# Performance work log

Measured on AMD Instinct MI355X. Metric: run time of the kernel, lower is better.

Reference implementation:

```python
import jax, jax.numpy as jnp
import numpy as np

NEG_FILL = jnp.finfo(jnp.float32).min  # stands in for tf.float64.min (overflows to -inf in f32)


def setup_inputs() -> dict:
    key = jax.random.key(0)
    k0, k1, k2, k3, k4 = jax.random.split(key, 5)
    B, N, E, D = 4, 4096, 1024, 256
    STD = 0.05  # tf.random_normal_initializer default stddev
    inputs = jax.random.normal(k0, (B, N, E), dtype=jnp.float32)
    Wq = STD * jax.random.normal(k1, (E, D), dtype=jnp.float32)
    Wk = STD * jax.random.normal(k2, (E, D), dtype=jnp.float32)
    Wvdown = STD * jax.random.normal(k3, (E, D), dtype=jnp.float32)
    Wvup = STD * jax.random.normal(k4, (D, E), dtype=jnp.float32)
    return {"inputs": inputs, "Wq": Wq, "Wk": Wk, "Wvdown": Wvdown, "Wvup": Wvup}


def reference(inputs, Wq, Wk, Wvdown, Wvup):
    B, N, E = inputs.shape
    D = Wq.shape[1]
    Q = inputs @ Wq                                   # [B, N, D]
    K = inputs @ Wk                                   # [B, N, D]
    score = jnp.einsum("bqd,bkd->bqk", Q, K)          # [B, N, N]
    score = score / jnp.sqrt(jnp.float32(D))
    # tf.linalg.band_part(score, -1, 0): keep lower triangle (causal)
    causal = jnp.tril(jnp.ones((N, N), dtype=bool))
    score = jnp.where(causal, score, 0.0)
    # original quirk: any exactly-zero entry (including masked ones) -> huge negative
    score = jnp.where(score != 0, score, NEG_FILL)
    attn = jax.nn.softmax(score, axis=-1)             # [B, N, N]
    V = inputs @ (Wvdown @ Wvup)                      # low-rank value proj, [B, N, E]
    return attn @ V                                   # [B, N, E]
```

## Files before the change

### kernel.cpp

```cpp
#include <hip/hip_runtime.h>
#include <hip/hip_bf16.h>


typedef __hip_bfloat16 bf16;
typedef __bf16 bf16x4 __attribute__((ext_vector_type(4)));
typedef __bf16 bf16x8 __attribute__((ext_vector_type(8)));
typedef float f32x4 __attribute__((ext_vector_type(4)));

#define BK 32
#define HALF_BYTES 8192

__device__ __forceinline__ void gload_lds16(const bf16* g, bf16* l) {
    __builtin_amdgcn_global_load_lds(
        (const __attribute__((address_space(1))) unsigned int*)g,
        (__attribute__((address_space(3))) unsigned int*)l, 16, 0, 0);
}

__device__ __forceinline__ void zero_acc(f32x4 acc[4][4]) {
#pragma unroll
    for (int mi = 0; mi < 4; ++mi)
#pragma unroll
        for (int ni = 0; ni < 4; ++ni) {
            f32x4 zf = {0.f, 0.f, 0.f, 0.f};
            acc[mi][ni] = zf;
        }
}

__device__ __forceinline__ void compute_step(const bf16* As, const bf16* Bs,
                                             int cur, int mrow, int nrow,
                                             int koff, f32x4 acc[4][4]) {
    const bf16* Ar = (const bf16*)((const char*)As + cur * HALF_BYTES);
    const bf16* Br = (const bf16*)((const char*)Bs + cur * HALF_BYTES);
    bf16x8 af[4], bfr[4];
#pragma unroll
    for (int mi = 0; mi < 4; ++mi)
        af[mi] = *(const bf16x8*)(Ar + (mrow + mi * 16) * BK + koff);
#pragma unroll
    for (int ni = 0; ni < 4; ++ni)
        bfr[ni] = *(const bf16x8*)(Br + (nrow + ni * 16) * BK + koff);
#pragma unroll
    for (int mi = 0; mi < 4; ++mi)
#pragma unroll
        for (int ni = 0; ni < 4; ++ni)
            acc[mi][ni] = __builtin_amdgcn_mfma_f32_16x16x32_bf16(
                af[mi], bfr[ni], acc[mi][ni], 0, 0, 0);
}

__device__ __forceinline__ void mm_tile(const bf16* __restrict__ Ablk,
                                        const bf16* __restrict__ Bblk,
                                        int lda, int ldb, int kiters,
                                        bf16* As, bf16* Bs, f32x4 acc[4][4]) {
    const int tid  = threadIdx.x;
    const int wave = tid >> 6;
    const int lane = tid & 63;

    const int F0 = wave * 2048 + lane * 16;
    const int F1 = F0 + 1024;
    const int r0 = F0 >> 6, c0 = (F0 & 63) >> 1;
    const int r1 = F1 >> 6, c1 = (F1 & 63) >> 1;
    const bf16* ga0 = Ablk + (size_t)r0 * lda + c0;
    const bf16* ga1 = Ablk + (size_t)r1 * lda + c1;
    const bf16* gb0 = Bblk + (size_t)r0 * ldb + c0;
    const bf16* gb1 = Bblk + (size_t)r1 * ldb + c1;

    const int waveM = wave >> 1, waveN = wave & 1;
    const int mrow = waveM * 64 + (lane & 15);
    const int nrow = waveN * 64 + (lane & 15);
    const int koff = (lane >> 4) * 8;

    gload_lds16(ga0, (bf16*)((char*)As + F0));
    gload_lds16(ga1, (bf16*)((char*)As + F1));
    gload_lds16(gb0, (bf16*)((char*)Bs + F0));
    gload_lds16(gb1, (bf16*)((char*)Bs + F1));
    ga0 += BK; ga1 += BK; gb0 += BK; gb1 += BK;

    int cur = 0;
    for (int it = 0; it < kiters - 1; ++it) {
        const int nxt = cur ^ 1;
        char* Ad = (char*)As + nxt * HALF_BYTES;
        char* Bd = (char*)Bs + nxt * HALF_BYTES;
        gload_lds16(ga0, (bf16*)(Ad + F0));
        gload_lds16(ga1, (bf16*)(Ad + F1));
        gload_lds16(gb0, (bf16*)(Bd + F0));
        gload_lds16(gb1, (bf16*)(Bd + F1));
        ga0 += BK; ga1 += BK; gb0 += BK; gb1 += BK;

        __builtin_amdgcn_sched_barrier(0);
        asm volatile("s_waitcnt vmcnt(4)" ::: "memory");
        __builtin_amdgcn_sched_barrier(0);
        __builtin_amdgcn_s_barrier();
        __builtin_amdgcn_sched_barrier(0);

        compute_step(As, Bs, cur, mrow, nrow, koff, acc);

        __builtin_amdgcn_sched_barrier(0);
        asm volatile("s_waitcnt lgkmcnt(0)" ::: "memory");
        __builtin_amdgcn_sched_barrier(0);
        __builtin_amdgcn_s_barrier();
        __builtin_amdgcn_sched_barrier(0);
        cur = nxt;
    }

    __builtin_amdgcn_sched_barrier(0);
    asm volatile("s_waitcnt vmcnt(0)" ::: "memory");
    __builtin_amdgcn_sched_barrier(0);
    __builtin_amdgcn_s_barrier();
    __builtin_amdgcn_sched_barrier(0);
    compute_step(As, Bs, cur, mrow, nrow, koff, acc);
}

__global__ __launch_bounds__(256, 2) void k_gemm_plain(
    const bf16* __restrict__ A, long long aBatch,
    const bf16* __restrict__ BT, long long bBatch,
    bf16* __restrict__ C, long long cBatch,
    int lda, int ldb, int ldc, int kiters) {
    __shared__ __align__(16) bf16 As[2 * 128 * BK];
    __shared__ __align__(16) bf16 Bs[2 * 128 * BK];
    const int nBase = blockIdx.x * 128;
    const int mBase = blockIdx.y * 128;
    const int z = blockIdx.z;
    const bf16* Ab = A + (size_t)z * aBatch + (size_t)mBase * lda;
    const bf16* Bb = BT + (size_t)z * bBatch + (size_t)nBase * ldb;

    f32x4 acc[4][4];
    zero_acc(acc);
    mm_tile(Ab, Bb, lda, ldb, kiters, As, Bs, acc);

    const int tid = threadIdx.x, wave = tid >> 6, lane = tid & 63;
    const int waveM = wave >> 1, waveN = wave & 1;
    const int quad = lane >> 4, cno = lane & 15;
    bf16* Cb = C + (size_t)z * cBatch;
#pragma unroll
    for (int mi = 0; mi < 4; ++mi) {
        int row0 = mBase + waveM * 64 + mi * 16 + quad * 4;
#pragma unroll
        for (int ni = 0; ni < 4; ++ni) {
            int col = nBase + waveN * 64 + ni * 16 + cno;
#pragma unroll
            for (int r = 0; r < 4; ++r)
                Cb[(size_t)(row0 + r) * ldc + col] = __float2bfloat16(acc[mi][ni][r]);
        }
    }
}

#define P_BATCH 8650752ll
__global__ __launch_bounds__(256, 2) void k_score(
    const bf16* __restrict__ Qm, const bf16* __restrict__ Km,
    bf16* __restrict__ P, float* __restrict__ lsum) {
    const int f = blockIdx.x, b = blockIdx.z;
    int qt = (int)((sqrtf(8.f * (float)f + 1.f) - 1.f) * 0.5f);
    while ((qt + 1) * (qt + 2) / 2 <= f) ++qt;
    while (qt * (qt + 1) / 2 > f) --qt;
    const int kt = f - qt * (qt + 1) / 2;

    __shared__ __align__(16) bf16 As[2 * 128 * BK];
    __shared__ __align__(16) bf16 Bs[2 * 128 * BK];

    const bf16* Ab = Qm + ((size_t)b * 4096 + (size_t)qt * 128) * 256;
    const bf16* Bb = Km + ((size_t)b * 4096 + (size_t)kt * 128) * 256;

    f32x4 acc[4][4];
    zero_acc(acc);
    mm_tile(Ab, Bb, 256, 256, 256 / BK, As, Bs, acc);

    const int tid = threadIdx.x, wave = tid >> 6, lane = tid & 63;
    const int waveM = wave >> 1, waveN = wave & 1;
    const int quad = lane >> 4, cno = lane & 15;
    const int pitch = (qt + 1) * 128;
    bf16* Pb = P + b * P_BATCH + (size_t)16384 * (qt * (qt + 1) / 2);
    float* lb = lsum + b * 4096;
#pragma unroll
    for (int mi = 0; mi < 4; ++mi) {
        const int lq0 = waveM * 64 + mi * 16 + quad * 4;
        float rs[4] = {0.f, 0.f, 0.f, 0.f};
#pragma unroll
        for (int ni = 0; ni < 4; ++ni) {
            const int cn = waveN * 64 + ni * 16 + cno;
            const int gk = kt * 128 + cn;
#pragma unroll
            for (int r = 0; r < 4; ++r) {
                const int gq = qt * 128 + lq0 + r;
                float s = acc[mi][ni][r] * 0.0625f;
                float p = (gk <= gq && s != 0.0f) ? __expf(s) : 0.0f;
                bf16 pb = __float2bfloat16(p);
                Pb[(size_t)(lq0 + r) * pitch + gk] = pb;
                rs[r] += __bfloat162float(pb);
            }
        }
#pragma unroll
        for (int r = 0; r < 4; ++r) {
            float v = rs[r];
            v += __shfl_xor(v, 1);
            v += __shfl_xor(v, 2);
            v += __shfl_xor(v, 4);
            v += __shfl_xor(v, 8);
            if (cno == 0) atomicAdd(&lb[qt * 128 + lq0 + r], v);
        }
    }
}

__global__ __launch_bounds__(256, 2) void k_pv(
    const bf16* __restrict__ P, const bf16* __restrict__ VT,
    const float* __restrict__ lsum, float* __restrict__ Out) {
    __shared__ __align__(16) bf16 As[2 * 128 * BK];
    __shared__ __align__(16) bf16 Bs[2 * 128 * BK];
    const int l = blockIdx.x;
    const int dv = l >> 7;
    const int w = l & 127;
    const int b = w >> 5;
    const int u = w & 31;
    const int x = u & 7;
    const int k = u >> 3;
    const int m = (k + (dv >> 1)) & 3;
    const int qt = (m == 0) ? x : (m == 1) ? (15 - x)
                 : (m == 2) ? (16 + x) : (31 - x);
    const int dvBase = dv * 128;
    const int tid = threadIdx.x, wave = tid >> 6, lane = tid & 63;
    const int waveM = wave >> 1, waveN = wave & 1;
    const int quad = lane >> 4, cno = lane & 15;

    const bf16* Bb = VT + ((size_t)b * 1024 + dvBase) * 4096;
    float* Ob = Out + (size_t)b * 4096 * 1024;
    const float* lb = lsum + b * 4096;

    const int pitch = (qt + 1) * 128;
    const bf16* Ab = P + b * P_BATCH + (size_t)16384 * (qt * (qt + 1) / 2);

    f32x4 acc[4][4];
    zero_acc(acc);
    mm_tile(Ab, Bb, pitch, 4096, (qt + 1) * (128 / BK), As, Bs, acc);

#pragma unroll
    for (int mi = 0; mi < 4; ++mi) {
        const int lq0 = waveM * 64 + mi * 16 + quad * 4;
#pragma unroll
        for (int r = 0; r < 4; ++r) {
            const int gq = qt * 128 + lq0 + r;
            const float inv = 1.0f / lb[gq];
#pragma unroll
            for (int ni = 0; ni < 4; ++ni) {
                const int col = dvBase + waveN * 64 + ni * 16 + cno;
                Ob[(size_t)gq * 1024 + col] = acc[mi][ni][r] * inv;
            }
        }
    }
}

__global__ void k_cast(const float4* __restrict__ in, bf16* __restrict__ out,
                       int n4) {
    int i = blockIdx.x * 256 + threadIdx.x;
    if (i >= n4) return;
    float4 v = in[i];
    bf16x4 o;
    o[0] = (__bf16)v.x; o[1] = (__bf16)v.y; o[2] = (__bf16)v.z; o[3] = (__bf16)v.w;
    *(bf16x4*)(out + 4 * (size_t)i) = o;
}

__global__ void k_transpose(const float* __restrict__ in, bf16* __restrict__ out,
                            int n, int mask, int shift, int tstride) {
    int idx = blockIdx.x * 256 + threadIdx.x;
    if (idx >= n) return;
    out[idx] = __float2bfloat16(in[(size_t)(idx & mask) * tstride + (idx >> shift)]);
}

extern "C" void kernel_launch(void* const* d_in, const int* in_sizes, int n_in,
                              void* d_out, int out_size, void* d_ws, size_t ws_size,
                              hipStream_t stream) {
    const int B = 4, N = 4096, E = 1024, D = 256;
    const float* X   = (const float*)d_in[0];
    const float* Wq  = (const float*)d_in[1];
    const float* Wk  = (const float*)d_in[2];
    const float* Wvd = (const float*)d_in[3];
    const float* Wvu = (const float*)d_in[4];
    float* out = (float*)d_out;

    const long long MiB = 1ll << 20;
    char* ws = (char*)d_ws;
    bf16* Xb     = (bf16*)(ws);
    bf16* WqT    = (bf16*)(ws + 32 * MiB);
    bf16* WkT    = (bf16*)(ws + 32 * MiB + 524288);
    bf16* WvdT   = (bf16*)(ws + 32 * MiB + 1048576);
    bf16* WvupT  = (bf16*)(ws + 32 * MiB + 1572864);
    bf16* P      = (bf16*)(ws);
    bf16* Qm     = (bf16*)(ws + 66 * MiB);
    bf16* Km     = (bf16*)(ws + 74 * MiB);
    bf16* Vd     = (bf16*)(ws + 82 * MiB);
    bf16* VT     = (bf16*)(ws + 90 * MiB);
    float* lsum  = (float*)(ws + 122 * MiB);

    const int n4 = B * N * E / 4;
    k_cast<<<(n4 + 255) / 256, 256, 0, stream>>>((const float4*)X, Xb, n4);
    k_transpose<<<1024, 256, 0, stream>>>(Wq,  WqT,  E * D, 1023, 10, 256);
    k_transpose<<<1024, 256, 0, stream>>>(Wk,  WkT,  E * D, 1023, 10, 256);
    k_transpose<<<1024, 256, 0, stream>>>(Wvd, WvdT, E * D, 1023, 10, 256);
    k_transpose<<<1024, 256, 0, stream>>>(Wvu, WvupT, D * E, 255, 8, 1024);
    hipMemsetAsync(lsum, 0, (size_t)B * N * sizeof(float), stream);

    k_gemm_plain<<<dim3(D / 128, (B * N) / 128, 3), 256, 0, stream>>>(
        Xb, 0, WqT, (long long)D * E, Qm, (long long)B * N * D,
        E, E, D, E / BK);

    k_gemm_plain<<<dim3(N / 128, E / 128, B), 256, 0, stream>>>(
        WvupT, 0, Vd, (long long)N * D, VT, (long long)E * N,
        D, D, N, D / BK);

    k_score<<<dim3(528, 1, B), 256, 0, stream>>>(Qm, Km, P, lsum);

    k_pv<<<dim3(1024, 1, 1), 256, 0, stream>>>(P, VT, lsum, out);
}
```

Baseline: 331.6 us.

## Swizzle LDS tiles and add triple-buffered pipeline for PV GEMM

```diff
diff --git a/kernel.cpp b/kernel.cpp
--- a/kernel.cpp
+++ b/kernel.cpp
@@ -28,16 +28,16 @@
 
 __device__ __forceinline__ void compute_step(const bf16* As, const bf16* Bs,
                                              int cur, int mrow, int nrow,
-                                             int koff, f32x4 acc[4][4]) {
-    const bf16* Ar = (const bf16*)((const char*)As + cur * HALF_BYTES);
-    const bf16* Br = (const bf16*)((const char*)Bs + cur * HALF_BYTES);
+                                             int kswz, f32x4 acc[4][4]) {
+    const char* Ar = (const char*)As + cur * HALF_BYTES;
+    const char* Br = (const char*)Bs + cur * HALF_BYTES;
     bf16x8 af[4], bfr[4];
 #pragma unroll
     for (int mi = 0; mi < 4; ++mi)
-        af[mi] = *(const bf16x8*)(Ar + (mrow + mi * 16) * BK + koff);
+        af[mi] = *(const bf16x8*)(Ar + (mrow + mi * 16) * 64 + kswz);
 #pragma unroll
     for (int ni = 0; ni < 4; ++ni)
-        bfr[ni] = *(const bf16x8*)(Br + (nrow + ni * 16) * BK + koff);
+        bfr[ni] = *(const bf16x8*)(Br + (nrow + ni * 16) * 64 + kswz);
 #pragma unroll
     for (int mi = 0; mi < 4; ++mi)
 #pragma unroll
@@ -46,6 +46,7 @@
                 af[mi], bfr[ni], acc[mi][ni], 0, 0, 0);
 }
 
+template <int DEPTH>
 __device__ __forceinline__ void mm_tile(const bf16* __restrict__ Ablk,
                                         const bf16* __restrict__ Bblk,
                                         int lda, int ldb, int kiters,
@@ -56,8 +57,9 @@
 
     const int F0 = wave * 2048 + lane * 16;
     const int F1 = F0 + 1024;
-    const int r0 = F0 >> 6, c0 = (F0 & 63) >> 1;
-    const int r1 = F1 >> 6, c1 = (F1 & 63) >> 1;
+    const int r0 = F0 >> 6, r1 = F1 >> 6;
+    const int c0 = ((F0 & 63) ^ ((r0 & 3) << 4)) >> 1;
+    const int c1 = ((F1 & 63) ^ ((r1 & 3) << 4)) >> 1;
     const bf16* ga0 = Ablk + (size_t)r0 * lda + c0;
     const bf16* ga1 = Ablk + (size_t)r1 * lda + c1;
     const bf16* gb0 = Bblk + (size_t)r0 * ldb + c0;
@@ -66,39 +68,60 @@
     const int waveM = wave >> 1, waveN = wave & 1;
     const int mrow = waveM * 64 + (lane & 15);
     const int nrow = waveN * 64 + (lane & 15);
-    const int koff = (lane >> 4) * 8;
-
-    gload_lds16(ga0, (bf16*)((char*)As + F0));
-    gload_lds16(ga1, (bf16*)((char*)As + F1));
-    gload_lds16(gb0, (bf16*)((char*)Bs + F0));
-    gload_lds16(gb1, (bf16*)((char*)Bs + F1));
-    ga0 += BK; ga1 += BK; gb0 += BK; gb1 += BK;
+    const int kswz = (((lane >> 4) ^ (lane & 3)) << 4);
+
+#define STAGE_TO(buf)                                                        \
+    {                                                                        \
+        char* Ad = (char*)As + (buf) * HALF_BYTES;                           \
+        char* Bd = (char*)Bs + (buf) * HALF_BYTES;                           \
+        gload_lds16(ga0, (bf16*)(Ad + F0));                                  \
+        gload_lds16(ga1, (bf16*)(Ad + F1));                                  \
+        gload_lds16(gb0, (bf16*)(Bd + F0));                                  \
+        gload_lds16(gb1, (bf16*)(Bd + F1));                                  \
+        ga0 += BK; ga1 += BK; gb0 += BK; gb1 += BK;                          \
+    }
+
+    STAGE_TO(0);
+    if (DEPTH == 3) STAGE_TO(1);
 
     int cur = 0;
-    for (int it = 0; it < kiters - 1; ++it) {
-        const int nxt = cur ^ 1;
-        char* Ad = (char*)As + nxt * HALF_BYTES;
-        char* Bd = (char*)Bs + nxt * HALF_BYTES;
-        gload_lds16(ga0, (bf16*)(Ad + F0));
-        gload_lds16(ga1, (bf16*)(Ad + F1));
-        gload_lds16(gb0, (bf16*)(Bd + F0));
-        gload_lds16(gb1, (bf16*)(Bd + F1));
-        ga0 += BK; ga1 += BK; gb0 += BK; gb1 += BK;
-
+    int stg = DEPTH - 1;
+    for (int it = 0; it < kiters - (DEPTH - 1); ++it) {
+        STAGE_TO(stg);
+        stg = (stg + 1 == DEPTH) ? 0 : stg + 1;
+
+        __builtin_amdgcn_sched_barrier(0);
+        if constexpr (DEPTH == 2)
+            asm volatile("s_waitcnt vmcnt(4)" ::: "memory");
+        else
+            asm volatile("s_waitcnt vmcnt(8)" ::: "memory");
+        __builtin_amdgcn_sched_barrier(0);
+        __builtin_amdgcn_s_barrier();
+        __builtin_amdgcn_sched_barrier(0);
+
+        compute_step(As, Bs, cur, mrow, nrow, kswz, acc);
+
+        __builtin_amdgcn_sched_barrier(0);
+        asm volatile("s_waitcnt lgkmcnt(0)" ::: "memory");
+        __builtin_amdgcn_sched_barrier(0);
+        __builtin_amdgcn_s_barrier();
+        __builtin_amdgcn_sched_barrier(0);
+        cur = (cur + 1 == DEPTH) ? 0 : cur + 1;
+    }
+
+    if constexpr (DEPTH == 3) {
         __builtin_amdgcn_sched_barrier(0);
         asm volatile("s_waitcnt vmcnt(4)" ::: "memory");
         __builtin_amdgcn_sched_barrier(0);
         __builtin_amdgcn_s_barrier();
         __builtin_amdgcn_sched_barrier(0);
-
-        compute_step(As, Bs, cur, mrow, nrow, koff, acc);
-
+        compute_step(As, Bs, cur, mrow, nrow, kswz, acc);
         __builtin_amdgcn_sched_barrier(0);
         asm volatile("s_waitcnt lgkmcnt(0)" ::: "memory");
         __builtin_amdgcn_sched_barrier(0);
         __builtin_amdgcn_s_barrier();
         __builtin_amdgcn_sched_barrier(0);
-        cur = nxt;
+        cur = (cur + 1 == DEPTH) ? 0 : cur + 1;
     }
 
     __builtin_amdgcn_sched_barrier(0);
@@ -106,7 +129,8 @@
     __builtin_amdgcn_sched_barrier(0);
     __builtin_amdgcn_s_barrier();
     __builtin_amdgcn_sched_barrier(0);
-    compute_step(As, Bs, cur, mrow, nrow, koff, acc);
+    compute_step(As, Bs, cur, mrow, nrow, kswz, acc);
+#undef STAGE_TO
 }
 
 __global__ __launch_bounds__(256, 2) void k_gemm_plain(
@@ -124,7 +148,7 @@
 
     f32x4 acc[4][4];
     zero_acc(acc);
-    mm_tile(Ab, Bb, lda, ldb, kiters, As, Bs, acc);
+    mm_tile<2>(Ab, Bb, lda, ldb, kiters, As, Bs, acc);
 
     const int tid = threadIdx.x, wave = tid >> 6, lane = tid & 63;
     const int waveM = wave >> 1, waveN = wave & 1;
@@ -161,7 +185,7 @@
 
     f32x4 acc[4][4];
     zero_acc(acc);
-    mm_tile(Ab, Bb, 256, 256, 256 / BK, As, Bs, acc);
+    mm_tile<2>(Ab, Bb, 256, 256, 256 / BK, As, Bs, acc);
 
     const int tid = threadIdx.x, wave = tid >> 6, lane = tid & 63;
     const int waveM = wave >> 1, waveN = wave & 1;
@@ -202,8 +226,8 @@
 __global__ __launch_bounds__(256, 2) void k_pv(
     const bf16* __restrict__ P, const bf16* __restrict__ VT,
     const float* __restrict__ lsum, float* __restrict__ Out) {
-    __shared__ __align__(16) bf16 As[2 * 128 * BK];
-    __shared__ __align__(16) bf16 Bs[2 * 128 * BK];
+    __shared__ __align__(16) bf16 As[3 * 128 * BK];
+    __shared__ __align__(16) bf16 Bs[3 * 128 * BK];
     const int l = blockIdx.x;
     const int dv = l >> 7;
     const int w = l & 127;
@@ -228,7 +252,7 @@
 
     f32x4 acc[4][4];
     zero_acc(acc);
-    mm_tile(Ab, Bb, pitch, 4096, (qt + 1) * (128 / BK), As, Bs, acc);
+    mm_tile<3>(Ab, Bb, pitch, 4096, (qt + 1) * (128 / BK), As, Bs, acc);
 
 #pragma unroll
     for (int mi = 0; mi < 4; ++mi) {
```

New measurement: 369.1 us. +11.3%, slower.

## Load MFMA fragments directly from global memory in score and PV kernels

Applied to the files above, without the earlier changes.

```diff
diff --git a/kernel.cpp b/kernel.cpp
--- a/kernel.cpp
+++ b/kernel.cpp
@@ -26,24 +26,45 @@
         }
 }
 
-__device__ __forceinline__ void compute_step(const bf16* As, const bf16* Bs,
-                                             int cur, int mrow, int nrow,
-                                             int koff, f32x4 acc[4][4]) {
-    const bf16* Ar = (const bf16*)((const char*)As + cur * HALF_BYTES);
-    const bf16* Br = (const bf16*)((const char*)Bs + cur * HALF_BYTES);
-    bf16x8 af[4], bfr[4];
-#pragma unroll
-    for (int mi = 0; mi < 4; ++mi)
-        af[mi] = *(const bf16x8*)(Ar + (mrow + mi * 16) * BK + koff);
-#pragma unroll
-    for (int ni = 0; ni < 4; ++ni)
-        bfr[ni] = *(const bf16x8*)(Br + (nrow + ni * 16) * BK + koff);
-#pragma unroll
-    for (int mi = 0; mi < 4; ++mi)
-#pragma unroll
-        for (int ni = 0; ni < 4; ++ni)
-            acc[mi][ni] = __builtin_amdgcn_mfma_f32_16x16x32_bf16(
-                af[mi], bfr[ni], acc[mi][ni], 0, 0, 0);
+__device__ __forceinline__ void mm_tile_direct(const bf16* __restrict__ Ablk,
+                                               const bf16* __restrict__ Bblk,
+                                               int lda, int ldb, int kiters,
+                                               f32x4 acc[4][4]) {
+    const int tid  = threadIdx.x;
+    const int wave = tid >> 6;
+    const int lane = tid & 63;
+    const int waveM = wave >> 1, waveN = wave & 1;
+    const int mrow = waveM * 64 + (lane & 15);
+    const int nrow = waveN * 64 + (lane & 15);
+    const int koff = (lane >> 4) * 8;
+
+    const bf16* pa0 = Ablk + (size_t)(mrow +  0) * lda + koff;
+    const bf16* pa1 = Ablk + (size_t)(mrow + 16) * lda + koff;
+    const bf16* pa2 = Ablk + (size_t)(mrow + 32) * lda + koff;
+    const bf16* pa3 = Ablk + (size_t)(mrow + 48) * lda + koff;
+    const bf16* pb0 = Bblk + (size_t)(nrow +  0) * ldb + koff;
+    const bf16* pb1 = Bblk + (size_t)(nrow + 16) * ldb + koff;
+    const bf16* pb2 = Bblk + (size_t)(nrow + 32) * ldb + koff;
+    const bf16* pb3 = Bblk + (size_t)(nrow + 48) * ldb + koff;
+
+#pragma unroll 2
+    for (int it = 0; it < kiters; ++it) {
+        bf16x8 af[4], bfr[4];
+        af[0] = *(const bf16x8*)pa0; pa0 += BK;
+        af[1] = *(const bf16x8*)pa1; pa1 += BK;
+        af[2] = *(const bf16x8*)pa2; pa2 += BK;
+        af[3] = *(const bf16x8*)pa3; pa3 += BK;
+        bfr[0] = *(const bf16x8*)pb0; pb0 += BK;
+        bfr[1] = *(const bf16x8*)pb1; pb1 += BK;
+        bfr[2] = *(const bf16x8*)pb2; pb2 += BK;
+        bfr[3] = *(const bf16x8*)pb3; pb3 += BK;
+#pragma unroll
+        for (int mi = 0; mi < 4; ++mi)
+#pragma unroll
+            for (int ni = 0; ni < 4; ++ni)
+                acc[mi][ni] = __builtin_amdgcn_mfma_f32_16x16x32_bf16(
+                    af[mi], bfr[ni], acc[mi][ni], 0, 0, 0);
+    }
 }
 
 __device__ __forceinline__ void mm_tile(const bf16* __restrict__ Ablk,
@@ -68,22 +89,22 @@
     const int nrow = waveN * 64 + (lane & 15);
     const int koff = (lane >> 4) * 8;
 
-    gload_lds16(ga0, (bf16*)((char*)As + F0));
-    gload_lds16(ga1, (bf16*)((char*)As + F1));
-    gload_lds16(gb0, (bf16*)((char*)Bs + F0));
-    gload_lds16(gb1, (bf16*)((char*)Bs + F1));
-    ga0 += BK; ga1 += BK; gb0 += BK; gb1 += BK;
-
+#define STAGE_TO(buf)                                                        \
+    {                                                                        \
+        char* Ad = (char*)As + (buf) * HALF_BYTES;                           \
+        char* Bd = (char*)Bs + (buf) * HALF_BYTES;                           \
+        gload_lds16(ga0, (bf16*)(Ad + F0));                                  \
+        gload_lds16(ga1, (bf16*)(Ad + F1));                                  \
+        gload_lds16(gb0, (bf16*)(Bd + F0));                                  \
+        gload_lds16(gb1, (bf16*)(Bd + F1));                                  \
+        ga0 += BK; ga1 += BK; gb0 += BK; gb1 += BK;                          \
+    }
+
+    STAGE_TO(0);
     int cur = 0;
     for (int it = 0; it < kiters - 1; ++it) {
         const int nxt = cur ^ 1;
-        char* Ad = (char*)As + nxt * HALF_BYTES;
-        char* Bd = (char*)Bs + nxt * HALF_BYTES;
-        gload_lds16(ga0, (bf16*)(Ad + F0));
-        gload_lds16(ga1, (bf16*)(Ad + F1));
-        gload_lds16(gb0, (bf16*)(Bd + F0));
-        gload_lds16(gb1, (bf16*)(Bd + F1));
-        ga0 += BK; ga1 += BK; gb0 += BK; gb1 += BK;
+        STAGE_TO(nxt);
 
         __builtin_amdgcn_sched_barrier(0);
         asm volatile("s_waitcnt vmcnt(4)" ::: "memory");
@@ -91,7 +112,23 @@
         __builtin_amdgcn_s_barrier();
         __builtin_amdgcn_sched_barrier(0);
 
-        compute_step(As, Bs, cur, mrow, nrow, koff, acc);
+        {
+            const bf16* Ar = (const bf16*)((const char*)As + cur * HALF_BYTES);
+            const bf16* Br = (const bf16*)((const char*)Bs + cur * HALF_BYTES);
+            bf16x8 af[4], bfr[4];
+#pragma unroll
+            for (int mi = 0; mi < 4; ++mi)
+                af[mi] = *(const bf16x8*)(Ar + (mrow + mi * 16) * BK + koff);
+#pragma unroll
+            for (int ni = 0; ni < 4; ++ni)
+                bfr[ni] = *(const bf16x8*)(Br + (nrow + ni * 16) * BK + koff);
+#pragma unroll
+            for (int mi = 0; mi < 4; ++mi)
+#pragma unroll
+                for (int ni = 0; ni < 4; ++ni)
+                    acc[mi][ni] = __builtin_amdgcn_mfma_f32_16x16x32_bf16(
+                        af[mi], bfr[ni], acc[mi][ni], 0, 0, 0);
+        }
 
         __builtin_amdgcn_sched_barrier(0);
         asm volatile("s_waitcnt lgkmcnt(0)" ::: "memory");
@@ -106,7 +143,24 @@
     __builtin_amdgcn_sched_barrier(0);
     __builtin_amdgcn_s_barrier();
     __builtin_amdgcn_sched_barrier(0);
-    compute_step(As, Bs, cur, mrow, nrow, koff, acc);
+    {
+        const bf16* Ar = (const bf16*)((const char*)As + cur * HALF_BYTES);
+        const bf16* Br = (const bf16*)((const char*)Bs + cur * HALF_BYTES);
+        bf16x8 af[4], bfr[4];
+#pragma unroll
+        for (int mi = 0; mi < 4; ++mi)
+            af[mi] = *(const bf16x8*)(Ar + (mrow + mi * 16) * BK + koff);
+#pragma unroll
+        for (int ni = 0; ni < 4; ++ni)
+            bfr[ni] = *(const bf16x8*)(Br + (nrow + ni * 16) * BK + koff);
+#pragma unroll
+        for (int mi = 0; mi < 4; ++mi)
+#pragma unroll
+            for (int ni = 0; ni < 4; ++ni)
+                acc[mi][ni] = __builtin_amdgcn_mfma_f32_16x16x32_bf16(
+                    af[mi], bfr[ni], acc[mi][ni], 0, 0, 0);
+    }
+#undef STAGE_TO
 }
 
 __global__ __launch_bounds__(256, 2) void k_gemm_plain(
@@ -144,7 +198,7 @@
 }
 
 #define P_BATCH 8650752ll
-__global__ __launch_bounds__(256, 2) void k_score(
+__global__ __launch_bounds__(256, 4) void k_score(
     const bf16* __restrict__ Qm, const bf16* __restrict__ Km,
     bf16* __restrict__ P, float* __restrict__ lsum) {
     const int f = blockIdx.x, b = blockIdx.z;
@@ -153,15 +207,12 @@
     while (qt * (qt + 1) / 2 > f) --qt;
     const int kt = f - qt * (qt + 1) / 2;
 
-    __shared__ __align__(16) bf16 As[2 * 128 * BK];
-    __shared__ __align__(16) bf16 Bs[2 * 128 * BK];
-
     const bf16* Ab = Qm + ((size_t)b * 4096 + (size_t)qt * 128) * 256;
     const bf16* Bb = Km + ((size_t)b * 4096 + (size_t)kt * 128) * 256;
 
     f32x4 acc[4][4];
     zero_acc(acc);
-    mm_tile(Ab, Bb, 256, 256, 256 / BK, As, Bs, acc);
+    mm_tile_direct(Ab, Bb, 256, 256, 256 / BK, acc);
 
     const int tid = threadIdx.x, wave = tid >> 6, lane = tid & 63;
     const int waveM = wave >> 1, waveN = wave & 1;
@@ -199,11 +250,9 @@
     }
 }
 
-__global__ __launch_bounds__(256, 2) void k_pv(
+__global__ __launch_bounds__(256, 4) void k_pv(
     const bf16* __restrict__ P, const bf16* __restrict__ VT,
     const float* __restrict__ lsum, float* __restrict__ Out) {
-    __shared__ __align__(16) bf16 As[2 * 128 * BK];
-    __shared__ __align__(16) bf16 Bs[2 * 128 * BK];
     const int l = blockIdx.x;
     const int dv = l >> 7;
     const int w = l & 127;
@@ -228,7 +277,7 @@
 
     f32x4 acc[4][4];
     zero_acc(acc);
-    mm_tile(Ab, Bb, pitch, 4096, (qt + 1) * (128 / BK), As, Bs, acc);
+    mm_tile_direct(Ab, Bb, pitch, 4096, (qt + 1) * (128 / BK), acc);
 
 #pragma unroll
     for (int mi = 0; mi < 4; ++mi) {
```

New measurement: 514.1 us. 55.1% more time.
